# Kernel optimization log

Measured on AMD Instinct MI355X. Metric: run time of the kernel, lower is better.

The kernel has to match this reference:

```python
import jax, jax.numpy as jnp
import numpy as np

N_HEADS = 8
D_HEAD = 64
INNER = N_HEADS * D_HEAD  # 512
D_X = 512
D_CTX = 768

def setup_inputs() -> dict:
    key = jax.random.key(0)
    ks = jax.random.split(key, 7)
    x = jax.random.normal(ks[0], (4, 4096, D_X), dtype=jnp.float32)
    context = jax.random.normal(ks[1], (4, 1024, D_CTX), dtype=jnp.float32)
    # Glorot-ish scaled params
    Wq = jax.random.normal(ks[2], (D_X, INNER), dtype=jnp.float32) / np.sqrt(D_X)
    Wk = jax.random.normal(ks[3], (D_CTX, INNER), dtype=jnp.float32) / np.sqrt(D_CTX)
    Wv = jax.random.normal(ks[4], (D_CTX, INNER), dtype=jnp.float32) / np.sqrt(D_CTX)
    Wo = jax.random.normal(ks[5], (INNER, INNER), dtype=jnp.float32) / np.sqrt(INNER)
    bo = jnp.zeros((INNER,), dtype=jnp.float32)
    return {"x": x, "context": context, "Wq": Wq, "Wk": Wk, "Wv": Wv, "Wo": Wo, "bo": bo}

def reference(x, context, Wq, Wk, Wv, Wo, bo):
    B, Nq, _ = x.shape
    Nc = context.shape[1]
    scale = D_HEAD ** -0.5
    # QKV projections (no bias), reshape to heads: b s (h d) -> b h s d
    q = (x @ Wq).reshape(B, Nq, N_HEADS, D_HEAD).transpose(0, 2, 1, 3)
    k = (context @ Wk).reshape(B, Nc, N_HEADS, D_HEAD).transpose(0, 2, 1, 3)
    v = (context @ Wv).reshape(B, Nc, N_HEADS, D_HEAD).transpose(0, 2, 1, 3)
    # scores: [B, H, Nq, Nc]
    score = jnp.einsum('bhqd,bhkd->bhqk', q, k) * scale
    weights = jax.nn.softmax(score, axis=-1)
    attn = jnp.einsum('bhqk,bhkd->bhqd', weights, v)
    out = attn.transpose(0, 2, 1, 3).reshape(B, Nq, INNER)
    return out @ Wo + bo
```

## Files before the change

### kernel.cpp

```cpp
#include <hip/hip_runtime.h>
#include <math.h>

typedef __attribute__((ext_vector_type(8))) short s8v;
typedef __attribute__((ext_vector_type(4))) float f4v;
typedef unsigned short u16;
typedef unsigned int u32;

constexpr int Bsz = 4, NQ = 4096, NC = 1024, NH = 8, DH = 64, DI = 512, DC = 768;

__device__ __forceinline__ u16 f2bf(float f) {
  union { float f; u32 u; } v; v.f = f;
  u32 r = v.u + 0x7fff + ((v.u >> 16) & 1);
  return (u16)(r >> 16);
}

__device__ __forceinline__ u32 pack2(float a, float b) {
  union { float f; u32 u; } ua, ub; ua.f = a; ub.f = b;
#if __has_builtin(__builtin_amdgcn_perm)
  return __builtin_amdgcn_perm(ub.u + 0x8000u, ua.u + 0x8000u, 0x07060302u);
#else
  return ((ub.u + 0x8000u) & 0xffff0000u) | ((ua.u + 0x8000u) >> 16);
#endif
}

__device__ __forceinline__ u32 cvtpk(float a, float b) {
  u32 r;
  asm("v_cvt_pk_bf16_f32 %0, %1, %2" : "=v"(r) : "v"(a), "v"(b));
  return r;
}

#if __has_builtin(__builtin_amdgcn_exp2f)
#define EXP2(x) __builtin_amdgcn_exp2f(x)
#else
#define EXP2(x) exp2f(x)
#endif

__device__ __forceinline__ void g2l16(const void* g, void* l) {
  __builtin_amdgcn_global_load_lds((const __attribute__((address_space(1))) u32*)g,
                                   (__attribute__((address_space(3))) u32*)l, 16, 0, 0);
}

__global__ __launch_bounds__(256) void prep(const float* __restrict__ x, const float* __restrict__ ctx,
                                            const float* __restrict__ Wq, const float* __restrict__ Wk,
                                            const float* __restrict__ Wv, const float* __restrict__ Wo,
                                            u16* __restrict__ xb, u16* __restrict__ cb,
                                            u16* __restrict__ wqT, u16* __restrict__ wkvT,
                                            u16* __restrict__ woT) {
  int bx = blockIdx.x;
  if (bx < 11264) {
    const int NX4 = Bsz * NQ * DI / 4;
    const int NC4 = Bsz * NC * DC / 4;
    int i = bx * 256 + threadIdx.x;
    float4 v; u16* dst; int j;
    if (i < NX4) { v = ((const float4*)x)[i]; dst = xb; j = i; }
    else { j = i - NX4; if (j >= NC4) return; v = ((const float4*)ctx)[j]; dst = cb; }
    ushort4 o; o.x = f2bf(v.x); o.y = f2bf(v.y); o.z = f2bf(v.z); o.w = f2bf(v.w);
    ((ushort4*)dst)[j] = o;
    return;
  }
  int idx = bx - 11264;
  int z = idx / 96, rem = idx % 96, kx = rem % 12, ny = rem / 12;
  const float* src; u16* dst; int K; const int N = 512;
  if (z == 0)      { src = Wq; dst = wqT;              K = 512; }
  else if (z == 1) { src = Wk; dst = wkvT;             K = 768; }
  else if (z == 2) { src = Wv; dst = wkvT + 512 * 768; K = 768; }
  else             { src = Wo; dst = woT;              K = 512; }
  int k0 = kx * 64, n0 = ny * 64;
  if (k0 >= K) return;
  __shared__ u16 t[64][65];
  int tid = threadIdx.x, jr = tid & 63, ir = tid >> 6;
  for (int it = 0; it < 16; ++it) { int i = it * 4 + ir; t[i][jr] = f2bf(src[(size_t)(k0 + i) * N + n0 + jr]); }
  __syncthreads();
  for (int it = 0; it < 16; ++it) { int i = it * 4 + ir; dst[(size_t)(n0 + i) * K + k0 + jr] = t[jr][i]; }
}

template <int MODE>
__device__ __forceinline__ void gemm8p(const u16* __restrict__ A, const u16* __restrict__ Bt,
                                       void* __restrict__ C0, void* __restrict__ C1,
                                       const float* __restrict__ bias, int N, int K,
                                       float oscale, int nbx, int mby,
                                       u16* Ash, u16* Bsh) {
  int tid = threadIdx.x;
  int lane = tid & 63, quad = lane >> 4, l16 = lane & 15, wave = tid >> 6;
  int wm = (wave >> 2) * 64, wn = (wave & 3) * 64;
  int mb = mby * 128, nb = nbx * 256;
  int x7 = l16 & 7;
  f4v acc[4][4];
  #pragma unroll
  for (int i = 0; i < 4; i++)
    #pragma unroll
    for (int j = 0; j < 4; j++) acc[i][j] = (f4v){0.f, 0.f, 0.f, 0.f};

  int srow = tid >> 3;
  int sc = ((tid & 7) ^ (srow & 7)) * 8;
  const u16* Ap0 = A  + (size_t)(mb + srow) * K + sc;
  const u16* Bq0 = Bt + (size_t)(nb + srow) * K + sc;
  int lin = tid * 8;

#define SA(ts, dst) do { const u16* s_ = Ap0 + (size_t)(ts) * 64; \
    g2l16(s_, (dst) + lin); g2l16(s_ + (size_t)64 * K, (dst) + 4096 + lin); } while (0)
#define SB0(ts, dst) do { const u16* s_ = Bq0 + (size_t)(ts) * 64; \
    g2l16(s_, (dst) + lin); g2l16(s_ + (size_t)64 * K, (dst) + 4096 + lin); } while (0)
#define SB1(ts, dst) do { const u16* s_ = Bq0 + (size_t)(ts) * 64 + (size_t)128 * K; \
    g2l16(s_, (dst) + 8192 + lin); g2l16(s_ + (size_t)64 * K, (dst) + 12288 + lin); } while (0)

  int ak0 = ((0 + quad) ^ x7) * 8;
  int ak1 = ((4 + quad) ^ x7) * 8;

  s8v bfr[4];
#define PHASE(ABUF, BBUF, AKK, IP, LOADB, WAITN, ...) do { \
    if (LOADB) { \
      bfr[0] = *(const s8v*)((BBUF) + (wn +  0 + l16) * 64 + (AKK)); \
      bfr[1] = *(const s8v*)((BBUF) + (wn + 16 + l16) * 64 + (AKK)); \
      bfr[2] = *(const s8v*)((BBUF) + (wn + 32 + l16) * 64 + (AKK)); \
      bfr[3] = *(const s8v*)((BBUF) + (wn + 48 + l16) * 64 + (AKK)); \
    } \
    s8v af0 = *(const s8v*)((ABUF) + (wm + (IP) * 32 + l16) * 64 + (AKK)); \
    s8v af1 = *(const s8v*)((ABUF) + (wm + (IP) * 32 + 16 + l16) * 64 + (AKK)); \
    __VA_ARGS__; \
    { int wv_ = (WAITN); \
      if (wv_ == 6) asm volatile("s_waitcnt vmcnt(6)" ::: "memory"); \
      else if (wv_ == 0) asm volatile("s_waitcnt vmcnt(0)" ::: "memory"); } \
    asm volatile("" ::: "memory"); __builtin_amdgcn_s_barrier(); asm volatile("" ::: "memory"); \
    __builtin_amdgcn_s_setprio(1); \
    _Pragma("unroll") \
    for (int j = 0; j < 4; j++) { \
      acc[(IP)*2][j]   = __builtin_amdgcn_mfma_f32_16x16x32_bf16(af0, bfr[j], acc[(IP)*2][j],   0, 0, 0); \
      acc[(IP)*2+1][j] = __builtin_amdgcn_mfma_f32_16x16x32_bf16(af1, bfr[j], acc[(IP)*2+1][j], 0, 0, 0); \
    } \
    __builtin_amdgcn_s_setprio(0); \
    asm volatile("" ::: "memory"); __builtin_amdgcn_s_barrier(); asm volatile("" ::: "memory"); \
  } while (0)

  u16 *A0 = Ash, *A1 = Ash + 8192, *A2 = Ash + 16384;
  u16 *B0 = Bsh, *B1 = Bsh + 16384, *B2 = Bsh + 32768;

  SA(0, A0); SB0(0, B0); SB1(0, B0);
  SA(1, A1); SB0(1, B1); SB1(1, B1);
  asm volatile("s_waitcnt vmcnt(6)" ::: "memory");
  __builtin_amdgcn_s_barrier();
  asm volatile("" ::: "memory");

  int nkt = K >> 6;
  for (int t2 = 0; t2 < nkt; t2 += 2) {
    bool more = (t2 + 2 < nkt);
    PHASE(A0, B0, ak0, 0, true,  -1, if (more) SA(t2 + 2, A2));
    PHASE(A0, B0, ak0, 1, false, -1, if (more) SB0(t2 + 2, B2));
    PHASE(A0, B0, ak1, 0, true,  -1, if (more) SB1(t2 + 2, B2));
    PHASE(A0, B0, ak1, 1, false, (more ? 6 : 0), );
    PHASE(A1, B1, ak0, 0, true,  -1, if (more) SA(t2 + 3, A0));
    PHASE(A1, B1, ak0, 1, false, -1, if (more) SB0(t2 + 3, B0));
    PHASE(A1, B1, ak1, 0, true,  -1, if (more) SB1(t2 + 3, B0));
    PHASE(A1, B1, ak1, 1, false, (more ? 6 : -1), );
    u16* tA = A0; A0 = A2; A2 = A1; A1 = tA;
    u16* tB = B0; B0 = B2; B2 = B1; B1 = tB;
  }
#undef PHASE
#undef SA
#undef SB0
#undef SB1

  #pragma unroll
  for (int i = 0; i < 4; i++) {
    int rbase = mb + wm + i * 16 + quad * 4;
    #pragma unroll
    for (int j = 0; j < 4; j++) {
      int col = nb + wn + j * 16 + l16;
      if (MODE == 0) {
        u16* Cb = (u16*)C0;
        #pragma unroll
        for (int r = 0; r < 4; r++) Cb[(size_t)(rbase + r) * N + col] = f2bf(acc[i][j][r] * oscale);
      } else if (MODE == 1) {
        float* Cf = (float*)C0;
        #pragma unroll
        for (int r = 0; r < 4; r++) Cf[(size_t)(rbase + r) * N + col] = acc[i][j][r] + bias[col];
      } else {
        if (col < 512) {
          u16* Kb = (u16*)C0;
          #pragma unroll
          for (int r = 0; r < 4; r++) Kb[(size_t)(rbase + r) * 512 + col] = f2bf(acc[i][j][r]);
        } else {
          u16* Vt = (u16*)C1;
          int hd = col - 512, h = hd >> 6, d = hd & 63;
          int bb = rbase >> 10, tl = rbase & 1023;
          int tbase = tl & ~63, a0 = tl & 63;
          int pb = (a0 & 32) + ((a0 & 15) >> 2) * 8 + (((a0 >> 4) & 1) << 2);
          uint2 ov;
          ov.x = pack2(acc[i][j][0], acc[i][j][1]);
          ov.y = pack2(acc[i][j][2], acc[i][j][3]);
          *(uint2*)(Vt + ((size_t)(bb * NH + h) * DH + d) * NC + tbase + pb) = ov;
        }
      }
    }
  }
}

__global__ __launch_bounds__(512, 2) void proj_all(const u16* __restrict__ xb, const u16* __restrict__ cb,
                                                   const u16* __restrict__ wqT, const u16* __restrict__ wkvT,
                                                   u16* __restrict__ Qb, u16* __restrict__ Kb,
                                                   u16* __restrict__ Vtb, float qscale) {
  __shared__ alignas(16) u16 Ash[3 * 8192];
  __shared__ alignas(16) u16 Bsh[3 * 16384];
  int bx = blockIdx.x;
  if (bx < 128) {
    int bi = (bx & 7) * 16 + (bx >> 3);
    gemm8p<2>(cb, wkvT, Kb, Vtb, nullptr, 1024, 768, 1.0f, bi & 3, bi >> 2, Ash, Bsh);
  } else {
    int bq = bx - 128;
    int bi = (bq & 7) * 32 + (bq >> 3);
    gemm8p<0>(xb, wqT, Qb, nullptr, nullptr, 512, 512, qscale, bi & 1, bi >> 1, Ash, Bsh);
  }
}

__global__ __launch_bounds__(512, 2) void outproj(const u16* __restrict__ Ob, const u16* __restrict__ woT,
                                                  float* __restrict__ out, const float* __restrict__ bo) {
  __shared__ alignas(16) u16 Ash[3 * 8192];
  __shared__ alignas(16) u16 Bsh[3 * 16384];
  int bx = blockIdx.x;
  int bi = (bx & 7) * 32 + (bx >> 3);
  gemm8p<1>(Ob, woT, out, nullptr, bo, 512, 512, 1.0f, bi & 1, bi >> 1, Ash, Bsh);
}

__global__ __launch_bounds__(256, 2) void attn(const u16* __restrict__ Q, const u16* __restrict__ Kb,
                                               const u16* __restrict__ Vt, u16* __restrict__ O) {
  __shared__ alignas(16) u16 Kl[2][64][64];
  __shared__ alignas(16) u16 Vl[2][64][64];
  int qt = blockIdx.x, h = blockIdx.y, b = blockIdx.z;
  int tid = threadIdx.x, wave = tid >> 6, lane = tid & 63, quad = lane >> 4, l16 = lane & 15;
  int q0 = qt * 256 + wave * 64;
  int x7 = l16 & 7;

  int kr = tid >> 3, kc = (tid & 7) ^ (kr & 7);
  const u16* kg = Kb + ((size_t)b * NC + kr) * 512 + h * DH + kc * 8;
  const u16* vg = Vt + ((size_t)(b * NH + h) * DH + kr) * NC + kc * 8;

#define ASTAGE(kt, buf) do { \
    const u16* kg_ = kg + (size_t)(kt) * 64 * 512; \
    const u16* vg_ = vg + (kt) * 64; \
    u16* kl_ = (u16*)Kl + (buf) * 4096; u16* vl_ = (u16*)Vl + (buf) * 4096; \
    g2l16(kg_,            kl_ + tid * 8); \
    g2l16(kg_ + 32 * 512, kl_ + (tid + 256) * 8); \
    g2l16(vg_,            vl_ + tid * 8); \
    g2l16(vg_ + 32 * NC,  vl_ + (tid + 256) * 8); } while (0)

  s8v aq[4][2];
  {
    const u16* Qp = Q + ((size_t)b * NQ + q0 + l16) * DI + h * DH + quad * 8;
    #pragma unroll
    for (int n = 0; n < 4; n++) {
      aq[n][0] = *(const s8v*)(Qp + (size_t)n * 16 * DI);
      aq[n][1] = *(const s8v*)(Qp + (size_t)n * 16 * DI + 32);
    }
  }
  s8v vones;
  #pragma unroll
  for (int i = 0; i < 8; i++) vones[i] = (short)0x3F80;

  f4v oacc[4][4];
  f4v lacc[4];
  #pragma unroll
  for (int d = 0; d < 4; d++)
    #pragma unroll
    for (int n = 0; n < 4; n++) oacc[d][n] = (f4v){0.f, 0.f, 0.f, 0.f};
  #pragma unroll
  for (int n = 0; n < 4; n++) lacc[n] = (f4v){0.f, 0.f, 0.f, 0.f};

  ASTAGE(0, 0);
  for (int kt = 0; kt < NC / 64; ++kt) {
    int buf = kt & 1;
    __syncthreads();
    if (kt + 1 < NC / 64) ASTAGE(kt + 1, buf ^ 1);
    const u16* kb = (const u16*)Kl + buf * 4096;
    const u16* vb = (const u16*)Vl + buf * 4096;

    f4v S0[2][4], S1[2][4];
    #pragma unroll
    for (int mi = 0; mi < 2; mi++)
      #pragma unroll
      for (int n = 0; n < 4; n++) { S0[mi][n] = (f4v){0.f,0.f,0.f,0.f}; S1[mi][n] = (f4v){0.f,0.f,0.f,0.f}; }
    __builtin_amdgcn_s_setprio(1);
    #pragma unroll
    for (int cd = 0; cd < 2; cd++) {
      int ch = ((4 * cd + quad) ^ x7) * 8;
      s8v k00 = *(const s8v*)(kb + (l16     ) * 64 + ch);
      s8v k01 = *(const s8v*)(kb + (l16 + 16) * 64 + ch);
      #pragma unroll
      for (int n = 0; n < 4; n++) {
        S0[0][n] = __builtin_amdgcn_mfma_f32_16x16x32_bf16(k00, aq[n][cd], S0[0][n], 0, 0, 0);
        S0[1][n] = __builtin_amdgcn_mfma_f32_16x16x32_bf16(k01, aq[n][cd], S0[1][n], 0, 0, 0);
      }
      s8v k10 = *(const s8v*)(kb + (l16 + 32) * 64 + ch);
      s8v k11 = *(const s8v*)(kb + (l16 + 48) * 64 + ch);
      #pragma unroll
      for (int n = 0; n < 4; n++) {
        S1[0][n] = __builtin_amdgcn_mfma_f32_16x16x32_bf16(k10, aq[n][cd], S1[0][n], 0, 0, 0);
        S1[1][n] = __builtin_amdgcn_mfma_f32_16x16x32_bf16(k11, aq[n][cd], S1[1][n], 0, 0, 0);
      }
    }
    __builtin_amdgcn_s_setprio(0);

    s8v pf0[4];
    #pragma unroll
    for (int n = 0; n < 4; n++) {
      float p00 = EXP2(S0[0][n][0]), p01 = EXP2(S0[0][n][1]), p02 = EXP2(S0[0][n][2]), p03 = EXP2(S0[0][n][3]);
      float p10 = EXP2(S0[1][n][0]), p11 = EXP2(S0[1][n][1]), p12 = EXP2(S0[1][n][2]), p13 = EXP2(S0[1][n][3]);
      union { u32 d[4]; s8v v; } u;
      u.d[0] = cvtpk(p00, p01); u.d[1] = cvtpk(p02, p03);
      u.d[2] = cvtpk(p10, p11); u.d[3] = cvtpk(p12, p13);
      pf0[n] = u.v;
    }
    __builtin_amdgcn_s_setprio(1);
    #pragma unroll
    for (int n = 0; n < 4; n++)
      lacc[n] = __builtin_amdgcn_mfma_f32_16x16x32_bf16(vones, pf0[n], lacc[n], 0, 0, 0);
    #pragma unroll
    for (int d = 0; d < 4; d++) {
      int ch = (quad ^ x7) * 8;
      s8v vf = *(const s8v*)(vb + (d * 16 + l16) * 64 + ch);
      #pragma unroll
      for (int n = 0; n < 4; n++)
        oacc[d][n] = __builtin_amdgcn_mfma_f32_16x16x32_bf16(vf, pf0[n], oacc[d][n], 0, 0, 0);
    }
    __builtin_amdgcn_s_setprio(0);

    s8v pf1[4];
    #pragma unroll
    for (int n = 0; n < 4; n++) {
      float p00 = EXP2(S1[0][n][0]), p01 = EXP2(S1[0][n][1]), p02 = EXP2(S1[0][n][2]), p03 = EXP2(S1[0][n][3]);
      float p10 = EXP2(S1[1][n][0]), p11 = EXP2(S1[1][n][1]), p12 = EXP2(S1[1][n][2]), p13 = EXP2(S1[1][n][3]);
      union { u32 d[4]; s8v v; } u;
      u.d[0] = cvtpk(p00, p01); u.d[1] = cvtpk(p02, p03);
      u.d[2] = cvtpk(p10, p11); u.d[3] = cvtpk(p12, p13);
      pf1[n] = u.v;
    }
    __builtin_amdgcn_s_setprio(1);
    #pragma unroll
    for (int n = 0; n < 4; n++)
      lacc[n] = __builtin_amdgcn_mfma_f32_16x16x32_bf16(vones, pf1[n], lacc[n], 0, 0, 0);
    #pragma unroll
    for (int d = 0; d < 4; d++) {
      int ch = ((4 + quad) ^ x7) * 8;
      s8v vf = *(const s8v*)(vb + (d * 16 + l16) * 64 + ch);
      #pragma unroll
      for (int n = 0; n < 4; n++)
        oacc[d][n] = __builtin_amdgcn_mfma_f32_16x16x32_bf16(vf, pf1[n], oacc[d][n], 0, 0, 0);
    }
    __builtin_amdgcn_s_setprio(0);
  }
#undef ASTAGE

  float inv[4];
  #pragma unroll
  for (int n = 0; n < 4; n++) inv[n] = 1.0f / lacc[n][0];

  #pragma unroll
  for (int d = 0; d < 4; d++)
    #pragma unroll
    for (int n = 0; n < 4; n++) {
      int q = q0 + n * 16 + l16;
      uint2 ov;
      ov.x = cvtpk(oacc[d][n][0] * inv[n], oacc[d][n][1] * inv[n]);
      ov.y = cvtpk(oacc[d][n][2] * inv[n], oacc[d][n][3] * inv[n]);
      *(uint2*)(O + ((size_t)b * NQ + q) * DI + h * DH + d * 16 + quad * 4) = ov;
    }
}

extern "C" void kernel_launch(void* const* d_in, const int* in_sizes, int n_in,
                              void* d_out, int out_size, void* d_ws, size_t ws_size,
                              hipStream_t stream) {
  const float* x   = (const float*)d_in[0];
  const float* ctx = (const float*)d_in[1];
  const float* Wq  = (const float*)d_in[2];
  const float* Wk  = (const float*)d_in[3];
  const float* Wv  = (const float*)d_in[4];
  const float* Wo  = (const float*)d_in[5];
  const float* bo  = (const float*)d_in[6];
  float* out = (float*)d_out;

  u16* w    = (u16*)d_ws;
  u16* xb   = w;
  u16* cb   = xb   + 8388608;
  u16* wqT  = cb   + 3145728;
  u16* wkvT = wqT  + 262144;
  u16* woT  = wkvT + 786432;
  u16* Qb   = woT  + 262144;
  u16* Kbuf = Qb   + 8388608;
  u16* Vtb  = Kbuf + 2097152;
  u16* Ob   = Vtb  + 2097152;

  const float qscale = 0.125f * 1.44269504f;

  prep<<<11648, 256, 0, stream>>>(x, ctx, Wq, Wk, Wv, Wo, xb, cb, wqT, wkvT, woT);
  proj_all<<<384, 512, 0, stream>>>(xb, cb, wqT, wkvT, Qb, Kbuf, Vtb, qscale);
  attn<<<dim3(16, 8, 4), 256, 0, stream>>>(Qb, Kbuf, Vtb, Ob);
  outproj<<<256, 512, 0, stream>>>(Ob, woT, out, bo);
}
```

Baseline: 179.8 us.

## Software-pipeline attention loop: overlap QK^T and softmax of next tile with PV

Restructures the attention inner loop so that the QK^T scores and exp/pack for tile k+1 are interleaved with the PV MFMAs for tile k. V gets a triple buffer in shared memory, and the P fragments are double-buffered in registers. The grid is also flattened to 1D with an XCD-aware block remap, so blocks sharing the same (b,h) K/V land on the same chiplet. The aim is to hide exp/VALU latency behind matrix work and improve L2 reuse, at the cost of higher register pressure and extra LDS.

New measurement: 177.8 us (median of 2 runs). No clear change (-1.1%).

```diff
diff --git a/kernel.cpp b/kernel.cpp
--- a/kernel.cpp
+++ b/kernel.cpp
@@ -224,24 +224,23 @@
 __global__ __launch_bounds__(256, 2) void attn(const u16* __restrict__ Q, const u16* __restrict__ Kb,
                                                const u16* __restrict__ Vt, u16* __restrict__ O) {
   __shared__ alignas(16) u16 Kl[2][64][64];
-  __shared__ alignas(16) u16 Vl[2][64][64];
-  int qt = blockIdx.x, h = blockIdx.y, b = blockIdx.z;
+  __shared__ alignas(16) u16 Vl[3][64][64];
+  int bx = blockIdx.x;
+  int bi = (bx & 7) * 64 + (bx >> 3);
+  int qt = bi & 15, h = (bi >> 4) & 7, b = bi >> 7;
   int tid = threadIdx.x, wave = tid >> 6, lane = tid & 63, quad = lane >> 4, l16 = lane & 15;
   int q0 = qt * 256 + wave * 64;
   int x7 = l16 & 7;
+  int cv0 = (quad ^ x7) * 8, cv1 = ((4 + quad) ^ x7) * 8;
 
   int kr = tid >> 3, kc = (tid & 7) ^ (kr & 7);
   const u16* kg = Kb + ((size_t)b * NC + kr) * 512 + h * DH + kc * 8;
   const u16* vg = Vt + ((size_t)(b * NH + h) * DH + kr) * NC + kc * 8;
 
-#define ASTAGE(kt, buf) do { \
-    const u16* kg_ = kg + (size_t)(kt) * 64 * 512; \
-    const u16* vg_ = vg + (kt) * 64; \
-    u16* kl_ = (u16*)Kl + (buf) * 4096; u16* vl_ = (u16*)Vl + (buf) * 4096; \
-    g2l16(kg_,            kl_ + tid * 8); \
-    g2l16(kg_ + 32 * 512, kl_ + (tid + 256) * 8); \
-    g2l16(vg_,            vl_ + tid * 8); \
-    g2l16(vg_ + 32 * NC,  vl_ + (tid + 256) * 8); } while (0)
+#define SK(kt, dst) do { const u16* s_ = kg + (size_t)(kt) * 64 * 512; \
+    g2l16(s_, (dst) + tid * 8); g2l16(s_ + 32 * 512, (dst) + (tid + 256) * 8); } while (0)
+#define SV(kt, dst) do { const u16* s_ = vg + (kt) * 64; \
+    g2l16(s_, (dst) + tid * 8); g2l16(s_ + 32 * NC, (dst) + (tid + 256) * 8); } while (0)
 
   s8v aq[4][2];
   {
@@ -265,89 +264,88 @@
   #pragma unroll
   for (int n = 0; n < 4; n++) lacc[n] = (f4v){0.f, 0.f, 0.f, 0.f};
 
-  ASTAGE(0, 0);
-  for (int kt = 0; kt < NC / 64; ++kt) {
-    int buf = kt & 1;
-    __syncthreads();
-    if (kt + 1 < NC / 64) ASTAGE(kt + 1, buf ^ 1);
-    const u16* kb = (const u16*)Kl + buf * 4096;
-    const u16* vb = (const u16*)Vl + buf * 4096;
-
-    f4v S0[2][4], S1[2][4];
-    #pragma unroll
-    for (int mi = 0; mi < 2; mi++)
-      #pragma unroll
-      for (int n = 0; n < 4; n++) { S0[mi][n] = (f4v){0.f,0.f,0.f,0.f}; S1[mi][n] = (f4v){0.f,0.f,0.f,0.f}; }
-    __builtin_amdgcn_s_setprio(1);
-    #pragma unroll
-    for (int cd = 0; cd < 2; cd++) {
-      int ch = ((4 * cd + quad) ^ x7) * 8;
-      s8v k00 = *(const s8v*)(kb + (l16     ) * 64 + ch);
-      s8v k01 = *(const s8v*)(kb + (l16 + 16) * 64 + ch);
-      #pragma unroll
-      for (int n = 0; n < 4; n++) {
-        S0[0][n] = __builtin_amdgcn_mfma_f32_16x16x32_bf16(k00, aq[n][cd], S0[0][n], 0, 0, 0);
-        S0[1][n] = __builtin_amdgcn_mfma_f32_16x16x32_bf16(k01, aq[n][cd], S0[1][n], 0, 0, 0);
-      }
-      s8v k10 = *(const s8v*)(kb + (l16 + 32) * 64 + ch);
-      s8v k11 = *(const s8v*)(kb + (l16 + 48) * 64 + ch);
-      #pragma unroll
-      for (int n = 0; n < 4; n++) {
-        S1[0][n] = __builtin_amdgcn_mfma_f32_16x16x32_bf16(k10, aq[n][cd], S1[0][n], 0, 0, 0);
-        S1[1][n] = __builtin_amdgcn_mfma_f32_16x16x32_bf16(k11, aq[n][cd], S1[1][n], 0, 0, 0);
-      }
-    }
-    __builtin_amdgcn_s_setprio(0);
-
-    s8v pf0[4];
-    #pragma unroll
-    for (int n = 0; n < 4; n++) {
-      float p00 = EXP2(S0[0][n][0]), p01 = EXP2(S0[0][n][1]), p02 = EXP2(S0[0][n][2]), p03 = EXP2(S0[0][n][3]);
-      float p10 = EXP2(S0[1][n][0]), p11 = EXP2(S0[1][n][1]), p12 = EXP2(S0[1][n][2]), p13 = EXP2(S0[1][n][3]);
-      union { u32 d[4]; s8v v; } u;
-      u.d[0] = cvtpk(p00, p01); u.d[1] = cvtpk(p02, p03);
-      u.d[2] = cvtpk(p10, p11); u.d[3] = cvtpk(p12, p13);
-      pf0[n] = u.v;
-    }
-    __builtin_amdgcn_s_setprio(1);
-    #pragma unroll
-    for (int n = 0; n < 4; n++)
-      lacc[n] = __builtin_amdgcn_mfma_f32_16x16x32_bf16(vones, pf0[n], lacc[n], 0, 0, 0);
-    #pragma unroll
-    for (int d = 0; d < 4; d++) {
-      int ch = (quad ^ x7) * 8;
-      s8v vf = *(const s8v*)(vb + (d * 16 + l16) * 64 + ch);
-      #pragma unroll
-      for (int n = 0; n < 4; n++)
-        oacc[d][n] = __builtin_amdgcn_mfma_f32_16x16x32_bf16(vf, pf0[n], oacc[d][n], 0, 0, 0);
-    }
-    __builtin_amdgcn_s_setprio(0);
-
-    s8v pf1[4];
-    #pragma unroll
-    for (int n = 0; n < 4; n++) {
-      float p00 = EXP2(S1[0][n][0]), p01 = EXP2(S1[0][n][1]), p02 = EXP2(S1[0][n][2]), p03 = EXP2(S1[0][n][3]);
-      float p10 = EXP2(S1[1][n][0]), p11 = EXP2(S1[1][n][1]), p12 = EXP2(S1[1][n][2]), p13 = EXP2(S1[1][n][3]);
-      union { u32 d[4]; s8v v; } u;
-      u.d[0] = cvtpk(p00, p01); u.d[1] = cvtpk(p02, p03);
-      u.d[2] = cvtpk(p10, p11); u.d[3] = cvtpk(p12, p13);
-      pf1[n] = u.v;
-    }
-    __builtin_amdgcn_s_setprio(1);
-    #pragma unroll
-    for (int n = 0; n < 4; n++)
-      lacc[n] = __builtin_amdgcn_mfma_f32_16x16x32_bf16(vones, pf1[n], lacc[n], 0, 0, 0);
-    #pragma unroll
-    for (int d = 0; d < 4; d++) {
-      int ch = ((4 + quad) ^ x7) * 8;
-      s8v vf = *(const s8v*)(vb + (d * 16 + l16) * 64 + ch);
-      #pragma unroll
-      for (int n = 0; n < 4; n++)
-        oacc[d][n] = __builtin_amdgcn_mfma_f32_16x16x32_bf16(vf, pf1[n], oacc[d][n], 0, 0, 0);
-    }
-    __builtin_amdgcn_s_setprio(0);
-  }
-#undef ASTAGE
+  u16 *kc_ = (u16*)Kl[0], *ks_ = (u16*)Kl[1];
+  u16 *vr_ = (u16*)Vl[0], *vc_ = (u16*)Vl[1], *vs_ = (u16*)Vl[2];
+
+#define QKC(Sa, roff) do { \
+    _Pragma("unroll") for (int mi = 0; mi < 2; mi++) \
+      _Pragma("unroll") for (int n = 0; n < 4; n++) Sa[mi][n] = (f4v){0.f,0.f,0.f,0.f}; \
+    __builtin_amdgcn_s_setprio(1); \
+    _Pragma("unroll") for (int cd = 0; cd < 2; cd++) { \
+      int ch = ((4 * cd + quad) ^ x7) * 8; \
+      s8v ka_ = *(const s8v*)(kc_ + ((roff) + l16) * 64 + ch); \
+      s8v kb_ = *(const s8v*)(kc_ + ((roff) + 16 + l16) * 64 + ch); \
+      _Pragma("unroll") for (int n = 0; n < 4; n++) { \
+        Sa[0][n] = __builtin_amdgcn_mfma_f32_16x16x32_bf16(ka_, aq[n][cd], Sa[0][n], 0, 0, 0); \
+        Sa[1][n] = __builtin_amdgcn_mfma_f32_16x16x32_bf16(kb_, aq[n][cd], Sa[1][n], 0, 0, 0); } } \
+    __builtin_amdgcn_s_setprio(0); } while (0)
+
+#define SM_SLICE(Sa, pfN, g) do { \
+    float p00 = EXP2(Sa[0][g][0]), p01 = EXP2(Sa[0][g][1]), p02 = EXP2(Sa[0][g][2]), p03 = EXP2(Sa[0][g][3]); \
+    float p10 = EXP2(Sa[1][g][0]), p11 = EXP2(Sa[1][g][1]), p12 = EXP2(Sa[1][g][2]), p13 = EXP2(Sa[1][g][3]); \
+    union { u32 d[4]; s8v v; } u_; \
+    u_.d[0] = cvtpk(p00, p01); u_.d[1] = cvtpk(p02, p03); \
+    u_.d[2] = cvtpk(p10, p11); u_.d[3] = cvtpk(p12, p13); \
+    pfN[g] = u_.v; } while (0)
+
+#define PV_D(d, PFO0, PFO1) do { \
+    __builtin_amdgcn_s_setprio(1); \
+    s8v vf0_ = *(const s8v*)(vr_ + ((d) * 16 + l16) * 64 + cv0); \
+    s8v vf1_ = *(const s8v*)(vr_ + ((d) * 16 + l16) * 64 + cv1); \
+    _Pragma("unroll") for (int n = 0; n < 4; n++) \
+      oacc[d][n] = __builtin_amdgcn_mfma_f32_16x16x32_bf16(vf0_, PFO0[n], oacc[d][n], 0, 0, 0); \
+    _Pragma("unroll") for (int n = 0; n < 4; n++) \
+      oacc[d][n] = __builtin_amdgcn_mfma_f32_16x16x32_bf16(vf1_, PFO1[n], oacc[d][n], 0, 0, 0); \
+    __builtin_amdgcn_s_setprio(0); } while (0)
+
+#define LACC(PFO0, PFO1) do { \
+    __builtin_amdgcn_s_setprio(1); \
+    _Pragma("unroll") for (int n = 0; n < 4; n++) \
+      lacc[n] = __builtin_amdgcn_mfma_f32_16x16x32_bf16(vones, PFO0[n], lacc[n], 0, 0, 0); \
+    _Pragma("unroll") for (int n = 0; n < 4; n++) \
+      lacc[n] = __builtin_amdgcn_mfma_f32_16x16x32_bf16(vones, PFO1[n], lacc[n], 0, 0, 0); \
+    __builtin_amdgcn_s_setprio(0); } while (0)
+
+#define BODY(PFO0, PFO1, PFN0, PFN1, KT) do { \
+    __syncthreads(); \
+    if ((KT) + 1 < 16) { SK((KT) + 1, ks_); SV((KT) + 1, vs_); } \
+    f4v S0_[2][4], S1_[2][4]; \
+    QKC(S0_, 0); \
+    PV_D(0, PFO0, PFO1); SM_SLICE(S0_, PFN0, 0); SM_SLICE(S0_, PFN0, 1); \
+    PV_D(1, PFO0, PFO1); SM_SLICE(S0_, PFN0, 2); SM_SLICE(S0_, PFN0, 3); \
+    QKC(S1_, 32); \
+    PV_D(2, PFO0, PFO1); SM_SLICE(S1_, PFN1, 0); SM_SLICE(S1_, PFN1, 1); \
+    PV_D(3, PFO0, PFO1); SM_SLICE(S1_, PFN1, 2); SM_SLICE(S1_, PFN1, 3); \
+    LACC(PFO0, PFO1); \
+    { u16* t_ = kc_; kc_ = ks_; ks_ = t_; \
+      u16* r_ = vr_; vr_ = vc_; vc_ = vs_; vs_ = r_; } } while (0)
+
+  s8v pfA0[4], pfA1[4], pfB0[4], pfB1[4];
+
+  SK(0, kc_); SV(0, vr_);
+  SK(1, ks_); SV(1, vc_);
+  __syncthreads();
+  {
+    f4v S0_[2][4], S1_[2][4];
+    QKC(S0_, 0); QKC(S1_, 32);
+    SM_SLICE(S0_, pfA0, 0); SM_SLICE(S0_, pfA0, 1); SM_SLICE(S0_, pfA0, 2); SM_SLICE(S0_, pfA0, 3);
+    SM_SLICE(S1_, pfA1, 0); SM_SLICE(S1_, pfA1, 1); SM_SLICE(S1_, pfA1, 2); SM_SLICE(S1_, pfA1, 3);
+  }
+  { u16* t_ = kc_; kc_ = ks_; ks_ = t_; }
+
+  for (int kt = 1; kt < 16; kt += 2) {
+    BODY(pfA0, pfA1, pfB0, pfB1, kt);
+    if (kt + 1 < 16) BODY(pfB0, pfB1, pfA0, pfA1, kt + 1);
+  }
+  PV_D(0, pfB0, pfB1); PV_D(1, pfB0, pfB1); PV_D(2, pfB0, pfB1); PV_D(3, pfB0, pfB1);
+  LACC(pfB0, pfB1);
+#undef BODY
+#undef LACC
+#undef PV_D
+#undef SM_SLICE
+#undef QKC
+#undef SK
+#undef SV
 
   float inv[4];
   #pragma unroll
@@ -392,6 +390,6 @@
 
   prep<<<11648, 256, 0, stream>>>(x, ctx, Wq, Wk, Wv, Wo, xb, cb, wqT, wkvT, woT);
   proj_all<<<384, 512, 0, stream>>>(xb, cb, wqT, wkvT, Qb, Kbuf, Vtb, qscale);
-  attn<<<dim3(16, 8, 4), 256, 0, stream>>>(Qb, Kbuf, Vtb, Ob);
+  attn<<<512, 256, 0, stream>>>(Qb, Kbuf, Vtb, Ob);
   outproj<<<256, 512, 0, stream>>>(Ob, woT, out, bo);
 }
```
